# Kernel tuning notes

Measured on AMD Instinct MI355X. Metric: run time of the kernel, lower is better.

The kernel has to match this reference:

```python
import jax, jax.numpy as jnp
import numpy as np

B, V, T, C, H = 2, 4, 512, 768, 12
HD = C // H          # head dim = 64
QD = H * HD          # q_dim = 768
EPS_RMS = 1e-5
EPS_LN = 1e-6


def rotate_two(x):
    # interleaved pair rotation: (x0,x1,x2,x3,...) -> (-x1,x0,-x3,x2,...)
    return jnp.reshape(jnp.concatenate((-1.0 * x[..., 1::2, None], x[..., ::2, None]), axis=-1), x.shape)


def layer_norm(x, scale, bias=None):
    mu = jnp.mean(x, axis=-1, keepdims=True)
    xc = x - mu
    var = jnp.mean(xc * xc, axis=-1, keepdims=True)
    y = xc * jax.lax.rsqrt(var + EPS_LN) * scale
    return y + bias if bias is not None else y


def rms_norm(x, alpha):
    # alpha has shape [H, HD], broadcasts over leading dims
    mag = jnp.sqrt(jnp.mean(x.astype(jnp.float32) ** 2, axis=-1, keepdims=True) + EPS_RMS).astype(x.dtype)
    return alpha * x / mag


def apply_rope(x, sc):
    # x: [B,V,T,H,HD], sc: [T,HD,2]
    cos = sc[None, None, :, None, :, 0]
    sin = sc[None, None, :, None, :, 1]
    return x * cos + rotate_two(x) * sin


def seg_attention(q, k, v, seg):
    # q,k,v: [N,S,H,D] fp32; seg: [N,S] int. bf16 qkv as in the original flash-attn call.
    qb, kb, vb = (t.astype(jnp.bfloat16) for t in (q, k, v))
    scale = 1.0 / np.sqrt(q.shape[-1]).astype(np.float32)
    scores = jnp.einsum('bqhd,bkhd->bhqk', qb, kb, preferred_element_type=jnp.float32) * scale
    same = (seg[:, None, :, None] == seg[:, None, None, :])  # [N,1,S,S]
    scores = jnp.where(same, scores, jnp.float32(-1e30))
    attn = jax.nn.softmax(scores, axis=-1)
    out = jnp.einsum('bhqk,bkhd->bqhd', attn.astype(jnp.bfloat16), vb, preferred_element_type=jnp.float32)
    return out.astype(q.dtype)


def setup_inputs() -> dict:
    key = jax.random.key(0)
    ks = jax.random.split(key, 16)
    x = jax.random.normal(ks[0], (B, V, T, C), dtype=jnp.float32)
    patch_ids = jnp.sort(jax.random.randint(ks[1], (B, T), 0, 8), axis=-1).astype(jnp.int32)
    # standard RoPE table, pairs repeated to match rotate_two's interleaved layout
    inv_freq = 1.0 / (10000.0 ** (np.arange(0, HD, 2, dtype=np.float32) / HD))
    ang = np.arange(T, dtype=np.float32)[:, None] * inv_freq[None, :]       # [T, HD/2]
    cos = np.repeat(np.cos(ang), 2, axis=-1)                                 # [T, HD]
    sin = np.repeat(np.sin(ang), 2, axis=-1)
    sincos_rope = jnp.asarray(np.stack([cos, sin], axis=-1), dtype=jnp.float32)  # [T,HD,2]
    s = 0.02
    return {
        'x': x,
        'patch_ids': patch_ids,
        'sincos_rope': sincos_rope,
        'ln1_scale': jnp.ones((C,), jnp.float32),
        'w_qkv': jax.random.normal(ks[2], (C, 6 * QD), jnp.float32) * s,
        'rms_q_alpha': jnp.ones((H, HD), jnp.float32),
        'rms_k_alpha': jnp.ones((H, HD), jnp.float32),
        'rms_qs_alpha': jnp.ones((H, HD), jnp.float32),
        'rms_ks_alpha': jnp.ones((H, HD), jnp.float32),
        'w_out': jax.random.normal(ks[3], (2 * QD, C), jnp.float32) * s,
        'b_out': jax.random.normal(ks[4], (C,), jnp.float32) * 1e-6,
        'ls1_alpha': jnp.full((C,), 0.01, jnp.float32),
        'ln2_scale': jnp.ones((C,), jnp.float32),
        'ln2_bias': jnp.zeros((C,), jnp.float32),
        'w_mlp1': jax.random.normal(ks[5], (C, 4 * C), jnp.float32) * s,
        'b_mlp1': jax.random.normal(ks[6], (4 * C,), jnp.float32) * 1e-6,
        'w_mlp2': jax.random.normal(ks[7], (4 * C, C), jnp.float32) * s,
        'b_mlp2': jax.random.normal(ks[8], (C,), jnp.float32) * 1e-6,
        'ls2_alpha': jnp.full((C,), 0.01, jnp.float32),
    }


def reference(x, patch_ids, sincos_rope, ln1_scale, w_qkv, rms_q_alpha, rms_k_alpha,
              rms_qs_alpha, rms_ks_alpha, w_out, b_out, ls1_alpha, ln2_scale, ln2_bias,
              w_mlp1, b_mlp1, w_mlp2, b_mlp2, ls2_alpha):
    x_in = layer_norm(x, ln1_scale)                       # [B,V,T,C]
    qkv = x_in @ w_qkv                                    # [B,V,T,6*QD]
    q, k, v, qs, ks, vs = [p.reshape(B, V, T, H, HD) for p in jnp.split(qkv, 6, axis=-1)]
    q = rms_norm(q, rms_q_alpha)
    k = rms_norm(k, rms_k_alpha)
    qs = rms_norm(qs, rms_qs_alpha)
    ks = rms_norm(ks, rms_ks_alpha)
    q, k = apply_rope(q, sincos_rope), apply_rope(k, sincos_rope)
    qs, ks = apply_rope(qs, sincos_rope), apply_rope(ks, sincos_rope)
    # global attention: views concatenated along sequence -> [B, V*T, H, HD]
    qg, kg, vg = (t.reshape(B, V * T, H, HD) for t in (q, k, v))
    seg_g = jnp.tile(patch_ids, (1, V))                   # [B, V*T]
    xg = seg_attention(qg, kg, vg, seg_g).reshape(B, V, T, QD)
    # self-view attention: views concatenated along batch -> [V*B, T, H, HD]
    qs_, ks_, vs_ = (t.transpose(1, 0, 2, 3, 4).reshape(V * B, T, H, HD) for t in (qs, ks, vs))
    seg_s = jnp.tile(patch_ids[None], (V, 1, 1)).reshape(V * B, T)
    xs = seg_attention(qs_, ks_, vs_, seg_s).reshape(V, B, T, QD).transpose(1, 0, 2, 3)
    x0 = jnp.concatenate((xg, xs), axis=-1) @ w_out + b_out
    x0 = ls1_alpha * x0 + x                               # LayerScale + residual
    x1 = jax.nn.gelu(layer_norm(x0, ln2_scale, ln2_bias))
    x1 = jax.nn.gelu(x1 @ w_mlp1 + b_mlp1) @ w_mlp2 + b_mlp2
    return ls2_alpha * x1 + x0
```

## Files before the change

### kernel.cpp

```cpp
#include <hip/hip_runtime.h>

#define DEVI __device__ __forceinline__

typedef __attribute__((ext_vector_type(8))) short short8;
typedef __attribute__((ext_vector_type(4))) float f32x4;
typedef unsigned short u16;

DEVI u16 f2bf(float f){
  unsigned int u = __float_as_uint(f);
  unsigned int r = (u + 0x7FFFu + ((u>>16)&1u)) >> 16;
  return (u16)r;
}
DEVI float bf2f(u16 h){ return __uint_as_float(((unsigned int)h)<<16); }

DEVI unsigned int cvt_pk_bf16(float a, float b){
  unsigned int r;
  asm("v_cvt_pk_bf16_f32 %0, %1, %2" : "=v"(r) : "v"(a), "v"(b));
  return r;
}

DEVI float gelu_f(float x){
  float x3 = x*x*x;
  float t = tanhf(0.7978845608028654f*(x + 0.044715f*x3));
  return 0.5f*x*(1.0f + t);
}

DEVI void async_cp16(const void* g, void* l){
  __builtin_amdgcn_global_load_lds(
      (const __attribute__((address_space(1))) unsigned int*)g,
      (__attribute__((address_space(3))) unsigned int*)l, 16, 0, 0);
}

DEVI void wtrans_body(const float* __restrict__ w, u16* __restrict__ wt,
                      int K, int N, int bx, int by, int tid){
  __shared__ float tile[32][33];
  int tn = bx*32, tk = by*32;
  int r = tid>>3, c4 = (tid&7)*4;
  float4 vv = *(const float4*)&w[(size_t)(tk+r)*N + tn + c4];
  tile[r][c4+0]=vv.x; tile[r][c4+1]=vv.y; tile[r][c4+2]=vv.z; tile[r][c4+3]=vv.w;
  __syncthreads();
  u16 o[4];
  #pragma unroll
  for (int j=0;j<4;j++) o[j] = f2bf(tile[c4+j][r]);
  unsigned long long pk = (unsigned long long)o[0] | ((unsigned long long)o[1]<<16)
                        | ((unsigned long long)o[2]<<32) | ((unsigned long long)o[3]<<48);
  *(unsigned long long*)&wt[(size_t)(tn+r)*K + tk + c4] = pk;
}

__global__ __launch_bounds__(256) void wtrans4_k(
    const float* __restrict__ w0, u16* __restrict__ o0,
    const float* __restrict__ w1, u16* __restrict__ o1,
    const float* __restrict__ w2, u16* __restrict__ o2,
    const float* __restrict__ w3, u16* __restrict__ o3)
{
  int bid = blockIdx.x, tid = threadIdx.x;
  if (bid < 3456){            wtrans_body(w0,o0, 768,4608, bid%144, bid/144, tid); }
  else if (bid < 4608){ int b=bid-3456; wtrans_body(w1,o1,1536, 768, b%24,  b/24,  tid); }
  else if (bid < 6912){ int b=bid-4608; wtrans_body(w2,o2, 768,3072, b%96,  b/96,  tid); }
  else               { int b=bid-6912; wtrans_body(w3,o3,3072, 768, b%24,  b/24,  tid); }
}

__global__ __launch_bounds__(256) void ln1_k(const float* __restrict__ x,
                                             const float* __restrict__ sc,
                                             u16* __restrict__ xin){
  int row = blockIdx.x, tid = threadIdx.x;
  const float* xr = x + (size_t)row*768;
  float v[3]; float s=0.f, ss=0.f;
  #pragma unroll
  for (int i=0;i<3;i++){ v[i]=xr[tid+i*256]; s+=v[i]; ss+=v[i]*v[i]; }
  #pragma unroll
  for (int m=1;m<=32;m<<=1){ s += __shfl_xor(s,m,64); ss += __shfl_xor(ss,m,64); }
  __shared__ float ls0[4], ls1_[4];
  int w = tid>>6;
  if ((tid&63)==0){ ls0[w]=s; ls1_[w]=ss; }
  __syncthreads();
  s = ls0[0]+ls0[1]+ls0[2]+ls0[3]; ss = ls1_[0]+ls1_[1]+ls1_[2]+ls1_[3];
  float mu = s*(1.f/768.f);
  float var = ss*(1.f/768.f) - mu*mu;
  float inv = rsqrtf(var + 1e-6f);
  #pragma unroll
  for (int i=0;i<3;i++){ int c=tid+i*256; xin[(size_t)row*768+c] = f2bf((v[i]-mu)*inv*sc[c]); }
}

template<int EPI, int SPLITK>
__global__ __launch_bounds__(256) void gemm_k(
    const u16* __restrict__ A, const u16* __restrict__ Bt,
    int M, int N, int K,
    float* __restrict__ Cf, u16* __restrict__ Cb,
    const float* __restrict__ bias)
{
  __shared__ __align__(16) u16 Al[128*64];
  __shared__ __align__(16) u16 Bl[128*64];
  const int tid = threadIdx.x, w = tid>>6, l = tid&63;
  const int m0 = blockIdx.y*128, n0 = blockIdx.x*128;
  const int Ksub = K/SPLITK;
  const int kc = (SPLITK>1) ? blockIdx.z : 0;
  const int kbase = kc*Ksub;
  const int wr = (w>>1)*64, wc = (w&1)*64;
  f32x4 acc[4][4];
  #pragma unroll
  for (int i=0;i<4;i++)
    #pragma unroll
    for (int j=0;j<4;j++){ f32x4 z={0.f,0.f,0.f,0.f}; acc[i][j]=z; }
  const int srow0 = tid>>3, sc16 = tid&7;
  for (int k0=0; k0<Ksub; k0+=64){
    __syncthreads();
    #pragma unroll
    for (int it=0; it<4; ++it){
      int row = it*32 + srow0;
      int sc = sc16 ^ (row&7);
      async_cp16(A  + (size_t)(m0+row)*K + kbase + k0 + sc*8, &Al[(it*256+tid)*8]);
      async_cp16(Bt + (size_t)(n0+row)*K + kbase + k0 + sc*8, &Bl[(it*256+tid)*8]);
    }
    __syncthreads();
    #pragma unroll
    for (int ks=0; ks<2; ++ks){
      short8 af[4], bfr[4];
      #pragma unroll
      for (int mi=0;mi<4;++mi){
        int row = wr + mi*16 + (l&15);
        int boff = row*128 + (((l>>4)*16 + ks*64) ^ ((row&7)<<4));
        af[mi] = *(const short8*)((const char*)&Al[0] + boff);
      }
      #pragma unroll
      for (int ni=0;ni<4;++ni){
        int row = wc + ni*16 + (l&15);
        int boff = row*128 + (((l>>4)*16 + ks*64) ^ ((row&7)<<4));
        bfr[ni] = *(const short8*)((const char*)&Bl[0] + boff);
      }
      #pragma unroll
      for (int mi=0;mi<4;++mi)
        #pragma unroll
        for (int ni=0;ni<4;++ni)
          acc[mi][ni] = __builtin_amdgcn_mfma_f32_16x16x32_bf16(af[mi], bfr[ni], acc[mi][ni], 0,0,0);
    }
  }
  #pragma unroll
  for (int mi=0;mi<4;++mi){
    int rb = m0 + wr + mi*16 + ((l>>4)<<2);
    #pragma unroll
    for (int ni=0;ni<4;++ni){
      int col = n0 + wc + ni*16 + (l&15);
      #pragma unroll
      for (int r=0;r<4;r++){
        int row = rb + r;
        float v = acc[mi][ni][r];
        if (EPI==0)      Cf[((size_t)kc*M + row)*N + col] = v;
        else if (EPI==2) Cb[(size_t)row*N+col] = f2bf(gelu_f(v + bias[col]));
        else             Cb[(size_t)row*N+col] = f2bf(v);
      }
    }
  }
}

__global__ __launch_bounds__(256) void redln_k(
    const float* __restrict__ P, const float* __restrict__ bias,
    const float* __restrict__ lsc, const float* __restrict__ resid,
    const float* __restrict__ ln2sc, const float* __restrict__ ln2bi,
    float* __restrict__ x0, u16* __restrict__ x1)
{
  const size_t MN = 4096ull*768;
  int row = blockIdx.x, tid = threadIdx.x;
  float v[3]; float s=0.f, ss=0.f;
  #pragma unroll
  for (int i=0;i<3;i++){
    int c = tid + i*256;
    size_t idx = (size_t)row*768 + c;
    float acc = P[idx] + P[MN+idx] + P[2*MN+idx] + P[3*MN+idx];
    float y = lsc[c]*(acc + bias[c]) + resid[idx];
    x0[idx] = y;
    v[i] = y; s += y; ss += y*y;
  }
  #pragma unroll
  for (int m=1;m<=32;m<<=1){ s += __shfl_xor(s,m,64); ss += __shfl_xor(ss,m,64); }
  __shared__ float ls0[4], ls1_[4];
  int w = tid>>6;
  if ((tid&63)==0){ ls0[w]=s; ls1_[w]=ss; }
  __syncthreads();
  s = ls0[0]+ls0[1]+ls0[2]+ls0[3]; ss = ls1_[0]+ls1_[1]+ls1_[2]+ls1_[3];
  float mu = s*(1.f/768.f);
  float var = ss*(1.f/768.f) - mu*mu;
  float inv = rsqrtf(var + 1e-6f);
  #pragma unroll
  for (int i=0;i<3;i++){
    int c = tid + i*256;
    float y = (v[i]-mu)*inv*ln2sc[c] + ln2bi[c];
    x1[(size_t)row*768 + c] = f2bf(gelu_f(y));
  }
}

__global__ __launch_bounds__(256) void red_k(
    const float* __restrict__ P, const float* __restrict__ bias,
    const float* __restrict__ lsc, const float* __restrict__ resid,
    float* __restrict__ out)
{
  const size_t MN = 4096ull*768;
  size_t i = ((size_t)blockIdx.x*256 + threadIdx.x)*4;
  int c = (int)(i % 768);
  float4 a0 = *(const float4*)&P[i];
  float4 a1 = *(const float4*)&P[MN+i];
  float4 a2 = *(const float4*)&P[2*MN+i];
  float4 a3 = *(const float4*)&P[3*MN+i];
  float4 bi = *(const float4*)&bias[c];
  float4 ls = *(const float4*)&lsc[c];
  float4 rs = *(const float4*)&resid[i];
  float4 o;
  o.x = ls.x*(a0.x+a1.x+a2.x+a3.x + bi.x) + rs.x;
  o.y = ls.y*(a0.y+a1.y+a2.y+a3.y + bi.y) + rs.y;
  o.z = ls.z*(a0.z+a1.z+a2.z+a3.z + bi.z) + rs.z;
  o.w = ls.w*(a0.w+a1.w+a2.w+a3.w + bi.w) + rs.w;
  *(float4*)&out[i] = o;
}

__global__ __launch_bounds__(256) void postproc2_k(
  const u16* __restrict__ qkv, const float* __restrict__ sincos,
  const float* __restrict__ aq, const float* __restrict__ ak,
  const float* __restrict__ aqs, const float* __restrict__ aks,
  u16* __restrict__ qg, u16* __restrict__ kg, u16* __restrict__ vg,
  u16* __restrict__ qsg, u16* __restrict__ ksg, u16* __restrict__ vsg)
{
  __shared__ u16 vt[2][64*66];
  const int bid = blockIdx.x;
  const int b = bid/384; int r0 = bid - b*384;
  const int v = r0/96;   int r1 = r0 - v*96;
  const int t6 = r1/12;  const int h = r1 - t6*12;
  const int T0 = t6*64;
  const int tid = threadIdx.x, w = tid>>6, l = tid&63;
  const int tq = l>>4, dq = l&15;
  const int m0 = b*2048 + v*512;
  const size_t gQbase = ((size_t)(b*12) + h)*2048 + v*512;
  const size_t sQbase = ((size_t)((v*2+b)*12) + h)*512;

  #pragma unroll
  for (int qi=0; qi<4; ++qi){
    const int tt = (qi<2) ? qi : qi+1;
    const float* al = (qi==0)?aq:(qi==1)?ak:(qi==2)?aqs:aks;
    float4 alv = *(const float4*)&al[h*64 + dq*4];
    u16* dst = (qi==0)?qg:(qi==1)?kg:(qi==2)?qsg:ksg;
    const size_t obase = (qi<2) ? gQbase : sQbase;
    #pragma unroll
    for (int it=0; it<4; ++it){
      const int t = T0 + w*16 + it*4 + tq;
      const u16* src = &qkv[(size_t)(m0+t)*4608 + tt*768 + h*64 + dq*4];
      ushort2 u01 = *(const ushort2*)src;
      ushort2 u23 = *(const ushort2*)(src+2);
      float x0=bf2f(u01.x), x1=bf2f(u01.y), x2=bf2f(u23.x), x3=bf2f(u23.y);
      float ss = x0*x0+x1*x1+x2*x2+x3*x3;
      #pragma unroll
      for (int mm=1;mm<=8;mm<<=1) ss += __shfl_xor(ss,mm,64);
      float rinv = rsqrtf(ss*(1.f/64.f) + 1e-5f);
      x0 *= alv.x*rinv; x1 *= alv.y*rinv; x2 *= alv.z*rinv; x3 *= alv.w*rinv;
      float4 cs01 = *(const float4*)&sincos[(size_t)(t*64 + dq*4)*2];
      float4 cs23 = *(const float4*)&sincos[(size_t)(t*64 + dq*4)*2 + 4];
      float y0 = x0*cs01.x - x1*cs01.y;
      float y1 = x1*cs01.z + x0*cs01.w;
      float y2 = x2*cs23.x - x3*cs23.y;
      float y3 = x3*cs23.z + x2*cs23.w;
      unsigned int lo = cvt_pk_bf16(y0, y1);
      unsigned int hi = cvt_pk_bf16(y2, y3);
      unsigned int* po = (unsigned int*)&dst[(obase + t)*64 + dq*4];
      po[0] = lo; po[1] = hi;
    }
  }

  #pragma unroll
  for (int vi=0; vi<2; ++vi){
    const int tt = (vi==0) ? 2 : 5;
    #pragma unroll
    for (int it=0; it<4; ++it){
      const int t = T0 + w*16 + it*4 + tq;
      const int tl = w*16 + it*4 + tq;
      const u16* src = &qkv[(size_t)(m0+t)*4608 + tt*768 + h*64 + dq*4];
      ushort2 u01 = *(const ushort2*)src;
      ushort2 u23 = *(const ushort2*)(src+2);
      unsigned int* pl = (unsigned int*)&vt[vi][tl*66 + dq*4];
      pl[0] = (unsigned int)u01.x | ((unsigned int)u01.y<<16);
      pl[1] = (unsigned int)u23.x | ((unsigned int)u23.y<<16);
    }
  }
  __syncthreads();
  {
    const size_t vgb = (((size_t)(b*12) + h)*64)*2048 + v*512 + T0 + l;
    #pragma unroll
    for (int i=0;i<16;++i){
      int d = w*16 + i;
      vg[vgb + (size_t)d*2048] = vt[0][l*66 + d];
    }
    const size_t vsb = (((size_t)((v*2+b)*12) + h)*64)*512 + T0 + l;
    #pragma unroll
    for (int i=0;i<16;++i){
      int d = w*16 + i;
      vsg[vsb + (size_t)d*512] = vt[1][l*66 + d];
    }
  }
}

__global__ __launch_bounds__(256) void attn7_k(
  const u16* __restrict__ Qg, const u16* __restrict__ Kg, const u16* __restrict__ Vtg,
  const u16* __restrict__ Qs, const u16* __restrict__ Ks, const u16* __restrict__ Vts,
  u16* __restrict__ Out, const int* __restrict__ pids)
{
  __shared__ __align__(16) u16 Kl[64*64];
  __shared__ __align__(16) u16 Vl[64*64];
  __shared__ __align__(16) u16 Pl[4][16*64];
  __shared__ unsigned long long amask_s;
  const int gid = blockIdx.x;
  const int xcd = gid & 7, idx = gid >> 3;
  const int lid = (idx < 96) ? xcd*96 + idx : 768 + xcd*96 + (idx - 96);
  const int tid = threadIdx.x, w = tid>>6, l = tid&63;
  const u16 *Q, *K, *Vt; const int* prow;
  int L, seq, h, qb, orow0, ocol;
  if (lid < 768){
    seq = lid/384; int rem2 = lid - seq*384; h = rem2>>5; qb = rem2&31;
    Q=Qg; K=Kg; Vt=Vtg; L=2048;
    prow = pids + seq*512; orow0 = seq*2048; ocol = h*64;
  } else {
    int g2 = lid - 768; seq = g2/96; int rem2 = g2 - seq*96; h = rem2>>3; qb = rem2&7;
    Q=Qs; K=Ks; Vt=Vts; L=512;
    prow = pids + (seq&1)*512; orow0 = (seq&1)*2048 + (seq>>1)*512; ocol = 768 + h*64;
  }
  const size_t base = ((size_t)(seq*12) + h)*(size_t)L*64;
  const int q0 = qb*64, tq0 = q0 & 511;
  short8 qf[2];
  const int qrow = q0 + w*16 + (l&15);
  #pragma unroll
  for (int s=0;s<2;s++) qf[s] = *(const short8*)&Q[base + (size_t)qrow*64 + s*32 + (l>>4)*8];
  const int qlo = prow[tq0], qhi = prow[tq0+63];
  int sq[4];
  #pragma unroll
  for (int r=0;r<4;r++) sq[r] = prow[tq0 + w*16 + (l>>4)*4 + r];
  float lsum[4]; f32x4 ao[4];
  #pragma unroll
  for (int r=0;r<4;r++) lsum[r]=0.f;
  #pragma unroll
  for (int d=0;d<4;d++){ f32x4 z={0.f,0.f,0.f,0.f}; ao[d]=z; }
  const int nk = L/64;
  bool act = false;
  if (tid < 64 && tid < nk){
    int tk0 = (tid*64)&511;
    act = (prow[tk0+63] >= qlo) && (prow[tk0] <= qhi);
  }
  unsigned long long bm = __ballot(act);
  if (tid==0) amask_s = bm;
  __syncthreads();
  unsigned long long rem = amask_s;
  int t = (int)(__ffsll((unsigned long long)rem)-1); rem &= rem-1;
  const int srow0 = tid>>3, sc16 = tid&7;
  while (true){
    const int k0 = t*64;
    __syncthreads();
    #pragma unroll
    for (int it=0; it<2; ++it){
      int row = it*32 + srow0;
      int sc = sc16 ^ (row&7);
      async_cp16(&K[base + (size_t)(k0+row)*64 + sc*8],        &Kl[(it*256+tid)*8]);
      async_cp16(&Vt[base + (size_t)row*(size_t)L + k0 + sc*8], &Vl[(it*256+tid)*8]);
    }
    __syncthreads();
    const int tk0 = (t*64) & 511;
    int skv[4];
    #pragma unroll
    for (int kb=0;kb<4;kb++) skv[kb] = prow[tk0 + kb*16 + (l&15)];
    f32x4 s4[4];
    #pragma unroll
    for (int kb=0;kb<4;kb++){
      const int krow = kb*16 + (l&15);
      f32x4 a = {0.f,0.f,0.f,0.f};
      #pragma unroll
      for (int s=0;s<2;s++){
        int boff = krow*128 + ((s*64 + (l>>4)*16) ^ ((krow&7)<<4));
        short8 kf = *(const short8*)((const char*)&Kl[0] + boff);
        a = __builtin_amdgcn_mfma_f32_16x16x32_bf16(qf[s], kf, a, 0,0,0);
      }
      s4[kb] = a;
    }
    #pragma unroll
    for (int kb=0;kb<4;kb++){
      float p0 = (skv[kb] == sq[0]) ? __expf(s4[kb][0]*0.125f) : 0.f;
      float p1 = (skv[kb] == sq[1]) ? __expf(s4[kb][1]*0.125f) : 0.f;
      float p2 = (skv[kb] == sq[2]) ? __expf(s4[kb][2]*0.125f) : 0.f;
      float p3 = (skv[kb] == sq[3]) ? __expf(s4[kb][3]*0.125f) : 0.f;
      lsum[0]+=p0; lsum[1]+=p1; lsum[2]+=p2; lsum[3]+=p3;
      unsigned int u01 = cvt_pk_bf16(p0, p1);
      unsigned int u23 = cvt_pk_bf16(p2, p3);
      int prw0 = (l>>4)*4;
      Pl[w][(prw0+0)*64 + (((kb*32 + (l&15)*2) ^ (((prw0+0)&7)<<4))>>1)] = (u16)u01;
      Pl[w][(prw0+1)*64 + (((kb*32 + (l&15)*2) ^ (((prw0+1)&7)<<4))>>1)] = (u16)(u01>>16);
      Pl[w][(prw0+2)*64 + (((kb*32 + (l&15)*2) ^ (((prw0+2)&7)<<4))>>1)] = (u16)u23;
      Pl[w][(prw0+3)*64 + (((kb*32 + (l&15)*2) ^ (((prw0+3)&7)<<4))>>1)] = (u16)(u23>>16);
    }
    short8 pa[2];
    #pragma unroll
    for (int s=0;s<2;s++)
      pa[s] = *(const short8*)&Pl[w][(l&15)*64 + (((s*64 + (l>>4)*16) ^ (((l&15)&7)<<4))>>1)];
    #pragma unroll
    for (int d=0;d<4;d++){
      const int vrow = d*16 + (l&15);
      #pragma unroll
      for (int s=0;s<2;s++){
        int boff = vrow*128 + ((s*64 + (l>>4)*16) ^ ((vrow&7)<<4));
        short8 vf = *(const short8*)((const char*)&Vl[0] + boff);
        ao[d] = __builtin_amdgcn_mfma_f32_16x16x32_bf16(pa[s], vf, ao[d], 0,0,0);
      }
    }
    if (!rem) break;
    t = (int)(__ffsll((unsigned long long)rem)-1); rem &= rem-1;
  }
  #pragma unroll
  for (int r=0;r<4;r++){
    #pragma unroll
    for (int m=1;m<=8;m<<=1) lsum[r] += __shfl_xor(lsum[r], m, 64);
    lsum[r] = 1.0f / lsum[r];
  }
  #pragma unroll
  for (int d=0;d<4;d++){
    unsigned int u01 = cvt_pk_bf16(ao[d][0]*lsum[0], ao[d][1]*lsum[1]);
    unsigned int u23 = cvt_pk_bf16(ao[d][2]*lsum[2], ao[d][3]*lsum[3]);
    int prw0 = (l>>4)*4, col = d*16 + (l&15);
    Pl[w][(prw0+0)*64 + col] = (u16)u01;
    Pl[w][(prw0+1)*64 + col] = (u16)(u01>>16);
    Pl[w][(prw0+2)*64 + col] = (u16)u23;
    Pl[w][(prw0+3)*64 + col] = (u16)(u23>>16);
  }
  __builtin_amdgcn_s_waitcnt(0);
  {
    int r16 = l&15, cchunk = (l>>4)*16;
    uint4 v0 = *(const uint4*)&Pl[w][r16*64 + cchunk];
    uint4 v1 = *(const uint4*)&Pl[w][r16*64 + cchunk + 8];
    size_t orow = (size_t)(orow0 + q0 + w*16 + r16)*1536 + ocol + cchunk;
    *(uint4*)&Out[orow]     = v0;
    *(uint4*)&Out[orow + 8] = v1;
  }
}

extern "C" void kernel_launch(void* const* d_in, const int* in_sizes, int n_in,
                              void* d_out, int out_size, void* d_ws, size_t ws_size,
                              hipStream_t stream) {
  const float* x      = (const float*)d_in[0];
  const int*   patch  = (const int*)d_in[1];
  const float* sincos = (const float*)d_in[2];
  const float* ln1s   = (const float*)d_in[3];
  const float* wqkv   = (const float*)d_in[4];
  const float* aq     = (const float*)d_in[5];
  const float* ak     = (const float*)d_in[6];
  const float* aqs    = (const float*)d_in[7];
  const float* aks    = (const float*)d_in[8];
  const float* wout   = (const float*)d_in[9];
  const float* bout   = (const float*)d_in[10];
  const float* ls1    = (const float*)d_in[11];
  const float* ln2s   = (const float*)d_in[12];
  const float* ln2b   = (const float*)d_in[13];
  const float* wm1    = (const float*)d_in[14];
  const float* bm1    = (const float*)d_in[15];
  const float* wm2    = (const float*)d_in[16];
  const float* bm2    = (const float*)d_in[17];
  const float* ls2    = (const float*)d_in[18];
  float* out = (float*)d_out;

  char* ws = (char*)d_ws;
  size_t off = 0;
  auto alloc = [&](size_t bytes)->void*{ void* p = ws + off; off += (bytes + 255) & ~(size_t)255; return p; };
  u16*  wqkvT = (u16*)alloc(4608ull*768*2);
  u16*  woutT = (u16*)alloc(768ull*1536*2);
  u16*  wm1T  = (u16*)alloc(3072ull*768*2);
  u16*  wm2T  = (u16*)alloc(768ull*3072*2);
  u16*  xin   = (u16*)alloc(4096ull*768*2);
  u16*  qkvb  = (u16*)alloc(4096ull*4608*2);
  u16*  qg    = (u16*)alloc(3145728ull*2);
  u16*  kg    = (u16*)alloc(3145728ull*2);
  u16*  vg    = (u16*)alloc(3145728ull*2);
  u16*  qsg   = (u16*)alloc(3145728ull*2);
  u16*  ksg   = (u16*)alloc(3145728ull*2);
  u16*  vsg   = (u16*)alloc(3145728ull*2);
  u16*  cat   = (u16*)alloc(4096ull*1536*2);
  float* x0   = (float*)alloc(4096ull*768*4);
  u16*  x1    = (u16*)alloc(4096ull*768*2);
  u16*  hbuf  = (u16*)alloc(4096ull*3072*2);
  float* P    = (float*)qkvb;

  dim3 b256(256);
  wtrans4_k<<<9216,b256,0,stream>>>(wqkv,wqkvT, wout,woutT, wm1,wm1T, wm2,wm2T);
  ln1_k<<<4096,b256,0,stream>>>(x, ln1s, xin);
  gemm_k<3,1><<<dim3(36,32),b256,0,stream>>>(xin, wqkvT, 4096, 4608, 768, nullptr, qkvb, nullptr);
  postproc2_k<<<768,b256,0,stream>>>(qkvb, sincos, aq, ak, aqs, aks, qg,kg,vg,qsg,ksg,vsg);
  attn7_k<<<1536,b256,0,stream>>>(qg,kg,vg, qsg,ksg,vsg, cat, patch);
  gemm_k<0,4><<<dim3(6,32,4),b256,0,stream>>>(cat, woutT, 4096, 768, 1536, P, nullptr, nullptr);
  redln_k<<<4096,b256,0,stream>>>(P, bout, ls1, x, ln2s, ln2b, x0, x1);
  gemm_k<2,1><<<dim3(24,32),b256,0,stream>>>(x1, wm1T, 4096, 3072, 768, nullptr, hbuf, bm1);
  gemm_k<0,4><<<dim3(6,32,4),b256,0,stream>>>(hbuf, wm2T, 4096, 768, 3072, P, nullptr, nullptr);
  red_k<<<3072,b256,0,stream>>>(P, bm2, ls2, x0, out);
}
```

Baseline: 228.7 us.

## Store split-K partials in bf16 and remap blocks for XCD locality

The split-K GEMM partial sums are now written and read back as bf16 instead of fp32, halving the traffic of the partial buffer that the reduction kernels consume. The split-K launch is flattened to a 1D grid, with block IDs remapped so that the blocks landing on each XCD share a contiguous set of M rows across N tiles and K chunks, aiming to improve L2 reuse. Rounding each partial to bf16 before summing adds precision loss to the output projection and the MLP2 results.

```diff
diff --git a/kernel.cpp b/kernel.cpp
--- a/kernel.cpp
+++ b/kernel.cpp
@@ -86,22 +86,27 @@
 __global__ __launch_bounds__(256) void gemm_k(
     const u16* __restrict__ A, const u16* __restrict__ Bt,
     int M, int N, int K,
-    float* __restrict__ Cf, u16* __restrict__ Cb,
-    const float* __restrict__ bias)
+    u16* __restrict__ Cb, const float* __restrict__ bias)
 {
   __shared__ __align__(16) u16 Al[128*64];
   __shared__ __align__(16) u16 Bl[128*64];
   const int tid = threadIdx.x, w = tid>>6, l = tid&63;
-  const int m0 = blockIdx.y*128, n0 = blockIdx.x*128;
+  int bx, by, kc;
+  if (SPLITK>1){
+    int id = blockIdx.x;
+    int xcd = id&7, j = id>>3;
+    bx = j%6; int rr = (j/6)&3; kc = j/24;
+    by = xcd*4 + rr;
+  } else { bx = blockIdx.x; by = blockIdx.y; kc = 0; }
+  const int m0 = by*128, n0 = bx*128;
   const int Ksub = K/SPLITK;
-  const int kc = (SPLITK>1) ? blockIdx.z : 0;
   const int kbase = kc*Ksub;
   const int wr = (w>>1)*64, wc = (w&1)*64;
   f32x4 acc[4][4];
   #pragma unroll
   for (int i=0;i<4;i++)
     #pragma unroll
-    for (int j=0;j<4;j++){ f32x4 z={0.f,0.f,0.f,0.f}; acc[i][j]=z; }
+    for (int j2=0;j2<4;j2++){ f32x4 z={0.f,0.f,0.f,0.f}; acc[i][j2]=z; }
   const int srow0 = tid>>3, sc16 = tid&7;
   for (int k0=0; k0<Ksub; k0+=64){
     __syncthreads();
@@ -145,7 +150,7 @@
       for (int r=0;r<4;r++){
         int row = rb + r;
         float v = acc[mi][ni][r];
-        if (EPI==0)      Cf[((size_t)kc*M + row)*N + col] = v;
+        if (EPI==0)      Cb[((size_t)kc*M + row)*N + col] = f2bf(v);
         else if (EPI==2) Cb[(size_t)row*N+col] = f2bf(gelu_f(v + bias[col]));
         else             Cb[(size_t)row*N+col] = f2bf(v);
       }
@@ -154,7 +159,7 @@
 }
 
 __global__ __launch_bounds__(256) void redln_k(
-    const float* __restrict__ P, const float* __restrict__ bias,
+    const u16* __restrict__ P, const float* __restrict__ bias,
     const float* __restrict__ lsc, const float* __restrict__ resid,
     const float* __restrict__ ln2sc, const float* __restrict__ ln2bi,
     float* __restrict__ x0, u16* __restrict__ x1)
@@ -166,7 +171,7 @@
   for (int i=0;i<3;i++){
     int c = tid + i*256;
     size_t idx = (size_t)row*768 + c;
-    float acc = P[idx] + P[MN+idx] + P[2*MN+idx] + P[3*MN+idx];
+    float acc = bf2f(P[idx]) + bf2f(P[MN+idx]) + bf2f(P[2*MN+idx]) + bf2f(P[3*MN+idx]);
     float y = lsc[c]*(acc + bias[c]) + resid[idx];
     x0[idx] = y;
     v[i] = y; s += y; ss += y*y;
@@ -190,25 +195,25 @@
 }
 
 __global__ __launch_bounds__(256) void red_k(
-    const float* __restrict__ P, const float* __restrict__ bias,
+    const u16* __restrict__ P, const float* __restrict__ bias,
     const float* __restrict__ lsc, const float* __restrict__ resid,
     float* __restrict__ out)
 {
   const size_t MN = 4096ull*768;
   size_t i = ((size_t)blockIdx.x*256 + threadIdx.x)*4;
   int c = (int)(i % 768);
-  float4 a0 = *(const float4*)&P[i];
-  float4 a1 = *(const float4*)&P[MN+i];
-  float4 a2 = *(const float4*)&P[2*MN+i];
-  float4 a3 = *(const float4*)&P[3*MN+i];
+  ushort4 a0 = *(const ushort4*)&P[i];
+  ushort4 a1 = *(const ushort4*)&P[MN+i];
+  ushort4 a2 = *(const ushort4*)&P[2*MN+i];
+  ushort4 a3 = *(const ushort4*)&P[3*MN+i];
   float4 bi = *(const float4*)&bias[c];
   float4 ls = *(const float4*)&lsc[c];
   float4 rs = *(const float4*)&resid[i];
   float4 o;
-  o.x = ls.x*(a0.x+a1.x+a2.x+a3.x + bi.x) + rs.x;
-  o.y = ls.y*(a0.y+a1.y+a2.y+a3.y + bi.y) + rs.y;
-  o.z = ls.z*(a0.z+a1.z+a2.z+a3.z + bi.z) + rs.z;
-  o.w = ls.w*(a0.w+a1.w+a2.w+a3.w + bi.w) + rs.w;
+  o.x = ls.x*(bf2f(a0.x)+bf2f(a1.x)+bf2f(a2.x)+bf2f(a3.x) + bi.x) + rs.x;
+  o.y = ls.y*(bf2f(a0.y)+bf2f(a1.y)+bf2f(a2.y)+bf2f(a3.y) + bi.y) + rs.y;
+  o.z = ls.z*(bf2f(a0.z)+bf2f(a1.z)+bf2f(a2.z)+bf2f(a3.z) + bi.z) + rs.z;
+  o.w = ls.w*(bf2f(a0.w)+bf2f(a1.w)+bf2f(a2.w)+bf2f(a3.w) + bi.w) + rs.w;
   *(float4*)&out[i] = o;
 }
 
@@ -476,17 +481,17 @@
   float* x0   = (float*)alloc(4096ull*768*4);
   u16*  x1    = (u16*)alloc(4096ull*768*2);
   u16*  hbuf  = (u16*)alloc(4096ull*3072*2);
-  float* P    = (float*)qkvb;
+  u16*  P     = qkvb;
 
   dim3 b256(256);
   wtrans4_k<<<9216,b256,0,stream>>>(wqkv,wqkvT, wout,woutT, wm1,wm1T, wm2,wm2T);
   ln1_k<<<4096,b256,0,stream>>>(x, ln1s, xin);
-  gemm_k<3,1><<<dim3(36,32),b256,0,stream>>>(xin, wqkvT, 4096, 4608, 768, nullptr, qkvb, nullptr);
+  gemm_k<3,1><<<dim3(36,32),b256,0,stream>>>(xin, wqkvT, 4096, 4608, 768, qkvb, nullptr);
   postproc2_k<<<768,b256,0,stream>>>(qkvb, sincos, aq, ak, aqs, aks, qg,kg,vg,qsg,ksg,vsg);
   attn7_k<<<1536,b256,0,stream>>>(qg,kg,vg, qsg,ksg,vsg, cat, patch);
-  gemm_k<0,4><<<dim3(6,32,4),b256,0,stream>>>(cat, woutT, 4096, 768, 1536, P, nullptr, nullptr);
+  gemm_k<0,4><<<768,b256,0,stream>>>(cat, woutT, 4096, 768, 1536, P, nullptr);
   redln_k<<<4096,b256,0,stream>>>(P, bout, ls1, x, ln2s, ln2b, x0, x1);
-  gemm_k<2,1><<<dim3(24,32),b256,0,stream>>>(x1, wm1T, 4096, 3072, 768, nullptr, hbuf, bm1);
-  gemm_k<0,4><<<dim3(6,32,4),b256,0,stream>>>(hbuf, wm2T, 4096, 768, 3072, P, nullptr, nullptr);
+  gemm_k<2,1><<<dim3(24,32),b256,0,stream>>>(x1, wm1T, 4096, 3072, 768, hbuf, bm1);
+  gemm_k<0,4><<<768,b256,0,stream>>>(hbuf, wm2T, 4096, 768, 3072, P, nullptr);
   red_k<<<3072,b256,0,stream>>>(P, bm2, ls2, x0, out);
 }
```

Result: faster. 203.1 us (-11.2%).
